# Kernel tuning notes

Hardware: AMD Instinct MI355X
Metric: run time of the kernel (lower is better)

The kernel has to match this reference:

```python
import jax, jax.numpy as jnp
import numpy as np

SEQ_LEN = 4096
HIDDEN = 1024
WINDOW = 64  # window_width D; gaussian std = D/2 (Luong local-p)


def setup_inputs() -> dict:
    key = jax.random.key(0)
    k1, k2, k3, k4 = jax.random.split(key, 4)
    scale = 1.0 / np.sqrt(HIDDEN)
    return {
        "source_hidden_states": jax.random.normal(k1, (16, SEQ_LEN, HIDDEN), jnp.float32),
        "target_hidden_state": jax.random.normal(k2, (16, HIDDEN), jnp.float32),
        "W_p": jax.random.normal(k3, (HIDDEN, HIDDEN), jnp.float32) * scale,
        "b_p": jnp.zeros((HIDDEN,), jnp.float32),
        "v_p": jax.random.normal(k4, (HIDDEN,), jnp.float32) * scale,
        "b_v": jnp.zeros((), jnp.float32),
    }


def reference(source_hidden_states, target_hidden_state, W_p, b_p, v_p, b_v):
    # Luong local-p attention, scaled-dot alignment, many-to-one context.
    B, S, H = source_hidden_states.shape
    t = target_hidden_state[:, None, :]  # [B,1,H]

    # predicted aligned position: p = S * sigmoid(v_p^T tanh(W_p h_t))
    hp = jnp.tanh(t @ W_p + b_p)                      # [B,1,H]
    p = jax.nn.sigmoid(hp @ v_p[:, None] + b_v) * S   # [B,1,1] -> squeeze
    p = p[:, :, 0]                                     # [B,1]

    # scaled dot score: sum_h(source * target) / sqrt(H)
    score = jnp.einsum("bsh,bh->bs", source_hidden_states, target_hidden_state)
    score = score * (1.0 / np.sqrt(float(H)))          # [B,S]
    attn = jax.nn.softmax(score, axis=-1)              # [B,S]

    # gaussian window around predicted position, std = D/2
    pos = jnp.arange(S, dtype=jnp.float32)[None, :]    # [1,S]
    sigma = WINDOW / 2.0
    gauss = jnp.exp(-jnp.square(pos - p) / (2.0 * sigma * sigma))  # [B,S]
    attn = attn * gauss

    # context vector
    context = jnp.einsum("bs,bsh->bh", attn, source_hidden_states)  # [B,H]
    return context
```

## Files before the change

### kernel.cpp

```cpp
#include <hip/hip_runtime.h>
#include <math.h>

#define HID 1024
#define SEQ 4096
#define NB 16
#define CHUNK 64
#define NCHUNK (SEQ / CHUNK)

typedef float floatx4 __attribute__((ext_vector_type(4)));

__global__ __launch_bounds__(256) void kA(const float* __restrict__ tgt,
                                          const float* __restrict__ Wp,
                                          const float* __restrict__ bp,
                                          const float* __restrict__ vp,
                                          double* __restrict__ pPart) {
  __shared__ float tl[HID];
  __shared__ double red[4][64];
  const int b = blockIdx.x;
  const int jseg = blockIdx.y;
  const int j0 = jseg * 64;
  const int tid = threadIdx.x;

  #pragma unroll
  for (int k = 0; k < 4; ++k) tl[tid + k * 256] = tgt[b * HID + tid + k * 256];
  __syncthreads();

  const int jl  = tid & 63;
  const int hp4 = tid >> 6;
  double a0 = 0.0, a1 = 0.0, a2 = 0.0, a3 = 0.0;
  const float* wcol = Wp + (size_t)(hp4 * 256) * HID + j0 + jl;
  const float* tq = tl + hp4 * 256;
  for (int i = 0; i < 256; i += 4) {
    a0 += (double)tq[i + 0] * (double)wcol[(size_t)(i + 0) * HID];
    a1 += (double)tq[i + 1] * (double)wcol[(size_t)(i + 1) * HID];
    a2 += (double)tq[i + 2] * (double)wcol[(size_t)(i + 2) * HID];
    a3 += (double)tq[i + 3] * (double)wcol[(size_t)(i + 3) * HID];
  }
  red[hp4][jl] = (a0 + a1) + (a2 + a3);
  __syncthreads();

  if (tid < 64) {
    double s = red[0][tid] + red[1][tid] + red[2][tid] + red[3][tid];
    double hpv = tanh(s + (double)bp[j0 + tid]);
    double val = hpv * (double)vp[j0 + tid];
    #pragma unroll
    for (int off = 32; off; off >>= 1) val += __shfl_xor(val, off);
    if (tid == 0) pPart[b * 16 + jseg] = val;
  }
}

__device__ __forceinline__ float4 nt_load4(const float* p) {
  floatx4 v = __builtin_nontemporal_load((const floatx4*)p);
  return make_float4(v.x, v.y, v.z, v.w);
}

__global__ __launch_bounds__(256) void kB(const float* __restrict__ src,
                                          const float* __restrict__ tgt,
                                          const double* __restrict__ pPart,
                                          const float* __restrict__ bv,
                                          float* __restrict__ zPart,
                                          float* __restrict__ ctxPart) {
  const int chunk = blockIdx.x;
  const int b = chunk >> 6;
  const int c = chunk & 63;
  const int s0 = c * CHUNK;
  const int tid = threadIdx.x;
  const int wave = tid >> 6;
  const int lane = tid & 63;

  double lg = (double)bv[0];
  #pragma unroll
  for (int i = 0; i < 16; ++i) lg += pPart[b * 16 + i];
  const float pb = (float)(4096.0 / (1.0 + exp(-lg)));

  float4 tf[4];
  const float4* tg4 = (const float4*)(tgt + b * HID);
  #pragma unroll
  for (int k = 0; k < 4; ++k) tf[k] = tg4[k * 64 + lane];

  float4 acc[4];
  #pragma unroll
  for (int k = 0; k < 4; ++k) acc[k] = make_float4(0.f, 0.f, 0.f, 0.f);
  float z = 0.f;

  const int srow0 = s0 + wave * 16;
  const float* base = src + ((size_t)b * SEQ + srow0) * HID;

  float4 x[2][4];
  #pragma unroll
  for (int k = 0; k < 4; ++k) x[0][k] = nt_load4(base + (k * 64 + lane) * 4);

  #pragma unroll
  for (int r = 0; r < 16; ++r) {
    const int cur = r & 1, nxt = cur ^ 1;
    if (r + 1 < 16) {
      #pragma unroll
      for (int k = 0; k < 4; ++k)
        x[nxt][k] = nt_load4(base + ((r + 1) * 256 + k * 64 + lane) * 4);
    }

    float dot = 0.f;
    #pragma unroll
    for (int k = 0; k < 4; ++k) {
      dot = fmaf(x[cur][k].x, tf[k].x, dot);
      dot = fmaf(x[cur][k].y, tf[k].y, dot);
      dot = fmaf(x[cur][k].z, tf[k].z, dot);
      dot = fmaf(x[cur][k].w, tf[k].w, dot);
    }
    #pragma unroll
    for (int off = 32; off; off >>= 1) dot += __shfl_xor(dot, off);

    const float w = expf(dot * 0.03125f);
    const float ds = (float)(srow0 + r) - pb;
    const float g = expf(ds * ds * (-1.0f / 2048.0f));
    z += w;
    const float wg = w * g;
    #pragma unroll
    for (int k = 0; k < 4; ++k) {
      acc[k].x = fmaf(wg, x[cur][k].x, acc[k].x);
      acc[k].y = fmaf(wg, x[cur][k].y, acc[k].y);
      acc[k].z = fmaf(wg, x[cur][k].z, acc[k].z);
      acc[k].w = fmaf(wg, x[cur][k].w, acc[k].w);
    }
  }

  __shared__ float lctx[4][HID];
  __shared__ float lz[4];
  #pragma unroll
  for (int k = 0; k < 4; ++k)
    *(float4*)&lctx[wave][k * 256 + lane * 4] = acc[k];
  if (lane == 0) lz[wave] = z;
  __syncthreads();

  float4 s4 = make_float4(0.f, 0.f, 0.f, 0.f);
  #pragma unroll
  for (int w2 = 0; w2 < 4; ++w2) {
    float4 v = *(const float4*)&lctx[w2][tid * 4];
    s4.x += v.x; s4.y += v.y; s4.z += v.z; s4.w += v.w;
  }
  ((float4*)ctxPart)[(size_t)chunk * 256 + tid] = s4;
  if (tid == 0) zPart[chunk] = lz[0] + lz[1] + lz[2] + lz[3];
}

__global__ __launch_bounds__(256) void kC(const float* __restrict__ zPart,
                                          const float* __restrict__ ctxPart,
                                          float* __restrict__ out) {
  const int b = blockIdx.x;
  const int tid = threadIdx.x;
  float Z = 0.f;
  for (int c = 0; c < NCHUNK; ++c) Z += zPart[b * NCHUNK + c];
  const float inv = 1.0f / Z;
  float4 s4 = make_float4(0.f, 0.f, 0.f, 0.f);
  const float4* cp = (const float4*)ctxPart;
  for (int c = 0; c < NCHUNK; ++c) {
    float4 v = cp[((size_t)(b * NCHUNK + c)) * 256 + tid];
    s4.x += v.x; s4.y += v.y; s4.z += v.z; s4.w += v.w;
  }
  ((float4*)out)[b * 256 + tid] =
      make_float4(s4.x * inv, s4.y * inv, s4.z * inv, s4.w * inv);
}

extern "C" void kernel_launch(void* const* d_in, const int* in_sizes, int n_in,
                              void* d_out, int out_size, void* d_ws, size_t ws_size,
                              hipStream_t stream) {
  const float* src = (const float*)d_in[0];
  const float* tgt = (const float*)d_in[1];
  const float* Wp  = (const float*)d_in[2];
  const float* bp  = (const float*)d_in[3];
  const float* vp  = (const float*)d_in[4];
  const float* bv  = (const float*)d_in[5];
  float* out = (float*)d_out;

  double* pPart  = (double*)d_ws;
  float* zPart   = (float*)((char*)d_ws + 4096);
  float* ctxPart = (float*)((char*)d_ws + 8192);

  kA<<<dim3(NB, 16), 256, 0, stream>>>(tgt, Wp, bp, vp, pPart);
  kB<<<NB * NCHUNK, 256, 0, stream>>>(src, tgt, pPart, bv, zPart, ctxPart);
  kC<<<NB, 256, 0, stream>>>(zPart, ctxPart, out);
}
```

Baseline: 69.22 us.

## Precompute gaussian weights, use fast exp, split dot chains, widen final reduction grid

```diff
diff --git a/kernel.cpp b/kernel.cpp
--- a/kernel.cpp
+++ b/kernel.cpp
@@ -73,17 +73,29 @@
   for (int i = 0; i < 16; ++i) lg += pPart[b * 16 + i];
   const float pb = (float)(4096.0 / (1.0 + exp(-lg)));
 
+  const int srow0 = s0 + wave * 16;
+
+  float gr[16];
+  #pragma unroll
+  for (int r = 0; r < 16; ++r) {
+    const float ds = (float)(srow0 + r) - pb;
+    gr[r] = __expf(ds * ds * (-1.0f / 2048.0f));
+  }
+
   float4 tf[4];
   const float4* tg4 = (const float4*)(tgt + b * HID);
   #pragma unroll
-  for (int k = 0; k < 4; ++k) tf[k] = tg4[k * 64 + lane];
+  for (int k = 0; k < 4; ++k) {
+    tf[k] = tg4[k * 64 + lane];
+    tf[k].x *= 0.03125f; tf[k].y *= 0.03125f;
+    tf[k].z *= 0.03125f; tf[k].w *= 0.03125f;
+  }
 
   float4 acc[4];
   #pragma unroll
   for (int k = 0; k < 4; ++k) acc[k] = make_float4(0.f, 0.f, 0.f, 0.f);
   float z = 0.f;
 
-  const int srow0 = s0 + wave * 16;
   const float* base = src + ((size_t)b * SEQ + srow0) * HID;
 
   float4 x[2][4];
@@ -99,22 +111,22 @@
         x[nxt][k] = nt_load4(base + ((r + 1) * 256 + k * 64 + lane) * 4);
     }
 
-    float dot = 0.f;
+    float d[4];
     #pragma unroll
     for (int k = 0; k < 4; ++k) {
-      dot = fmaf(x[cur][k].x, tf[k].x, dot);
-      dot = fmaf(x[cur][k].y, tf[k].y, dot);
-      dot = fmaf(x[cur][k].z, tf[k].z, dot);
-      dot = fmaf(x[cur][k].w, tf[k].w, dot);
+      float t0 = x[cur][k].x * tf[k].x;
+      t0 = fmaf(x[cur][k].y, tf[k].y, t0);
+      t0 = fmaf(x[cur][k].z, tf[k].z, t0);
+      t0 = fmaf(x[cur][k].w, tf[k].w, t0);
+      d[k] = t0;
     }
+    float dot = (d[0] + d[1]) + (d[2] + d[3]);
     #pragma unroll
     for (int off = 32; off; off >>= 1) dot += __shfl_xor(dot, off);
 
-    const float w = expf(dot * 0.03125f);
-    const float ds = (float)(srow0 + r) - pb;
-    const float g = expf(ds * ds * (-1.0f / 2048.0f));
+    const float w = __expf(dot);
     z += w;
-    const float wg = w * g;
+    const float wg = w * gr[r];
     #pragma unroll
     for (int k = 0; k < 4; ++k) {
       acc[k].x = fmaf(wg, x[cur][k].x, acc[k].x);
@@ -145,19 +157,28 @@
 __global__ __launch_bounds__(256) void kC(const float* __restrict__ zPart,
                                           const float* __restrict__ ctxPart,
                                           float* __restrict__ out) {
+  __shared__ float red[4][64];
   const int b = blockIdx.x;
+  const int hseg = blockIdx.y;
   const int tid = threadIdx.x;
-  float Z = 0.f;
-  for (int c = 0; c < NCHUNK; ++c) Z += zPart[b * NCHUNK + c];
-  const float inv = 1.0f / Z;
-  float4 s4 = make_float4(0.f, 0.f, 0.f, 0.f);
-  const float4* cp = (const float4*)ctxPart;
-  for (int c = 0; c < NCHUNK; ++c) {
-    float4 v = cp[((size_t)(b * NCHUNK + c)) * 256 + tid];
-    s4.x += v.x; s4.y += v.y; s4.z += v.z; s4.w += v.w;
-  }
-  ((float4*)out)[b * 256 + tid] =
-      make_float4(s4.x * inv, s4.y * inv, s4.z * inv, s4.w * inv);
+  const int col = tid & 63;
+  const int grp = tid >> 6;
+
+  float acc = 0.f;
+  #pragma unroll
+  for (int i = 0; i < 16; ++i) {
+    const int chunk = grp * 16 + i;
+    acc += ctxPart[((size_t)(b * NCHUNK + chunk)) * HID + hseg * 64 + col];
+  }
+  red[grp][col] = acc;
+  __syncthreads();
+
+  if (tid < 64) {
+    float Z = 0.f;
+    for (int c = 0; c < NCHUNK; ++c) Z += zPart[b * NCHUNK + c];
+    const float s = red[0][tid] + red[1][tid] + red[2][tid] + red[3][tid];
+    out[b * HID + hseg * 64 + tid] = s / Z;
+  }
 }
 
 extern "C" void kernel_launch(void* const* d_in, const int* in_sizes, int n_in,
@@ -177,5 +198,5 @@
 
   kA<<<dim3(NB, 16), 256, 0, stream>>>(tgt, Wp, bp, vp, pPart);
   kB<<<NB * NCHUNK, 256, 0, stream>>>(src, tgt, pPart, bv, zPart, ctxPart);
-  kC<<<NB, 256, 0, stream>>>(zPart, ctxPart, out);
-}
+  kC<<<dim3(NB, 16), 256, 0, stream>>>(zPart, ctxPart, out);
+}
```

Result: slower. 73.77 us (+6.6%).
